# Kernel optimization log

Measured on AMD Instinct MI355X. Metric: run time of the kernel, lower is better.

Reference implementation:

```python
import jax, jax.numpy as jnp
import numpy as np

B, T, D_IN, H, LAT = 256, 512, 32, 128, 64


def lstm_scan(x, Wih, Whh, bih, bhh):
    """PyTorch-convention single-layer LSTM over x [B,T,D] -> hidden states [B,T,H].
    Gate order: i, f, g, o. Gates = x@Wih.T + bih + h@Whh.T + bhh."""
    Bm, _, _ = x.shape
    Hm = Whh.shape[1]
    # precompute input contributions for all timesteps: [B,T,4H]
    xg = jnp.einsum('btd,gd->btg', x, Wih) + bih + bhh

    def step(carry, g_t):
        h, c = carry
        gates = g_t + h @ Whh.T  # [B,4H]
        i, f, g, o = jnp.split(gates, 4, axis=-1)
        i = jax.nn.sigmoid(i)
        f = jax.nn.sigmoid(f)
        g = jnp.tanh(g)
        o = jax.nn.sigmoid(o)
        c = f * c + i * g
        h = o * jnp.tanh(c)
        return (h, c), h

    h0 = jnp.zeros((Bm, Hm), x.dtype)
    (_, _), hs = jax.lax.scan(step, (h0, h0), jnp.swapaxes(xg, 0, 1))
    return jnp.swapaxes(hs, 0, 1)  # [B,T,H]


def setup_inputs() -> dict:
    key = jax.random.key(0)
    ks = jax.random.split(key, 14)
    s = 1.0 / np.sqrt(H)

    def u(k, shape):
        return jax.random.uniform(k, shape, jnp.float32, -s, s)

    return {
        'x': jax.random.normal(ks[0], (B, T, D_IN), jnp.float32),
        # encoder LSTM (input_dim -> hidden)
        'enc_Wih': u(ks[1], (4 * H, D_IN)),
        'enc_Whh': u(ks[2], (4 * H, H)),
        'enc_bih': u(ks[3], (4 * H,)),
        'enc_bhh': u(ks[4], (4 * H,)),
        # encoder linear (hidden -> latent)
        'enc_Wl': u(ks[5], (LAT, H)),
        'enc_bl': u(ks[6], (LAT,)),
        # decoder LSTM (latent -> hidden)
        'dec_Wih': u(ks[7], (4 * H, LAT)),
        'dec_Whh': u(ks[8], (4 * H, H)),
        'dec_bih': u(ks[9], (4 * H,)),
        'dec_bhh': u(ks[10], (4 * H,)),
        # decoder linear (hidden -> input_dim)
        'dec_Wl': u(ks[11], (D_IN, H)),
        'dec_bl': u(ks[12], (D_IN,)),
    }


def reference(x, enc_Wih, enc_Whh, enc_bih, enc_bhh, enc_Wl, enc_bl,
              dec_Wih, dec_Whh, dec_bih, dec_bhh, dec_Wl, dec_bl):
    # Encoder: last hidden state -> linear -> latent
    hs = lstm_scan(x, enc_Wih, enc_Whh, enc_bih, enc_bhh)  # [B,T,H]
    h_last = hs[:, -1]                                     # == hidden.squeeze(0)
    encoded = h_last @ enc_Wl.T + enc_bl                   # [B,LAT]
    # Decoder: repeat latent over time, LSTM, linear
    z = jnp.broadcast_to(encoded[:, None, :], (encoded.shape[0], T, encoded.shape[1]))
    hs2 = lstm_scan(z, dec_Wih, dec_Whh, dec_bih, dec_bhh)  # [B,T,H]
    decoded = hs2 @ dec_Wl.T + dec_bl                       # [B,T,D_IN]
    return encoded, decoded
```

## Files before the change

### kernel.cpp

```cpp
#include <hip/hip_runtime.h>

#define NB   256
#define NT   512
#define NDIN 32
#define NH   128
#define NLAT 64
#define HSTR 136

typedef float    f32x4 __attribute__((ext_vector_type(4)));
typedef _Float16 h2    __attribute__((ext_vector_type(2)));
typedef _Float16 h4    __attribute__((ext_vector_type(4)));

__device__ __forceinline__ float dot2(h2 a, h2 b, float c) {
  return __builtin_amdgcn_fdot2(a, b, c, false);
}
__device__ __forceinline__ h2 bc2(float v) { return __builtin_bit_cast(h2, v); }
__device__ __forceinline__ h2 pk2(float a, float b) { return h2{(_Float16)a, (_Float16)b}; }

#define NLOG2E 1.44269504f
__device__ __forceinline__ float tanh_f(float x) {
  float s = __builtin_amdgcn_rcpf(1.f + __builtin_amdgcn_exp2f(x * (-2.f * NLOG2E)));
  return fmaf(2.f, s, -1.f);
}

template <int CTRL>
__device__ __forceinline__ float dpp_mov(float v) {
  int p = __builtin_amdgcn_update_dpp(0, __builtin_bit_cast(int, v),
                                      CTRL, 0xF, 0xF, true);
  return __builtin_bit_cast(float, p);
}
#define QXOR1 0xB1
#define QXOR2 0x4E
#define QP1   0x39
#define QP2   0x4E
#define QP3   0x93
template <int CTRL>
__device__ __forceinline__ float qadd(float v) { return v + dpp_mov<CTRL>(v); }

__global__ __launch_bounds__(512, 1) void lstm_ae_kernel(
    const float* __restrict__ x,
    const float* __restrict__ eWih,
    const float* __restrict__ eWhh,
    const float* __restrict__ eBih,
    const float* __restrict__ eBhh,
    const float* __restrict__ eWl,
    const float* __restrict__ eBl,
    const float* __restrict__ dWih,
    const float* __restrict__ dWhh,
    const float* __restrict__ dBih,
    const float* __restrict__ dBhh,
    const float* __restrict__ dWl,
    const float* __restrict__ dBl,
    float* __restrict__ outE,
    float* __restrict__ outD)
{
  extern __shared__ __align__(16) char smem[];
  float*    encs = (float*)smem;
  _Float16* hs   = (_Float16*)(encs + NLAT);
  _Float16* hist = hs + 2 * NH;
  _Float16* xs   = hist;
  float*    gtmp = (float*)(hist + NT * HSTR);

  const int tid = threadIdx.x;
  const int b   = blockIdx.x;
  const int u   = tid >> 2;
  const int kc  = tid & 3;
  const bool writer = (kc == 0);
  const bool k0 = (kc & 1) != 0;
  const bool k1 = (kc & 2) != 0;
  const bool gth = (kc == 2);
  const float km = gth ? (-2.f * NLOG2E) : -NLOG2E;
  const float pa = gth ? 2.f : 1.f;
  const float pb = gth ? -1.f : 0.f;

  {
    const float4* xg = (const float4*)(x + (size_t)b * (NT * NDIN));
    h4* xo = (h4*)xs;
#pragma unroll
    for (int i = 0; i < 8; ++i) {
      int idx = i * 512 + tid;
      float4 v = xg[idx];
      xo[idx] = h4{(_Float16)v.x, (_Float16)v.y, (_Float16)v.z, (_Float16)v.w};
    }
  }

  h2 ew[64], dw[64], ewih[16];
  float binit[4];
#pragma unroll
  for (int g = 0; g < 4; ++g) {
    const int r = g * NH + u;
    const float4* p = (const float4*)(eWhh + (size_t)r * NH + 32 * kc);
#pragma unroll
    for (int j = 0; j < 8; ++j) {
      float4 v = p[j];
      ew[g * 16 + 2 * j]     = pk2(v.x, v.y);
      ew[g * 16 + 2 * j + 1] = pk2(v.z, v.w);
    }
    const float4* q = (const float4*)(eWih + (size_t)r * NDIN + 8 * kc);
    float4 v0 = q[0], v1 = q[1];
    ewih[g * 4 + 0] = pk2(v0.x, v0.y);
    ewih[g * 4 + 1] = pk2(v0.z, v0.w);
    ewih[g * 4 + 2] = pk2(v1.x, v1.y);
    ewih[g * 4 + 3] = pk2(v1.z, v1.w);
    float bsum = eBih[r] + eBhh[r];
    binit[g] = writer ? bsum : 0.f;
  }
  if (tid < 2 * NH) hs[tid] = (_Float16)0.f;
  float c = 0.f;
  __syncthreads();

#pragma unroll 1
  for (int t = 0; t < NT; ++t) {
    const float4* hp = (const float4*)(hs + (t & 1) * NH + 32 * kc);
    float4 h0 = hp[0], h1 = hp[1], h2v = hp[2], h3 = hp[3];
    float4 xv = *(const float4*)(xs + t * NDIN + 8 * kc);
    float zz[4];
#pragma unroll
    for (int g = 0; g < 4; ++g) {
      float A = binit[g];
      A = dot2(ew[g * 16 +  0], bc2(h0.x), A);
      A = dot2(ew[g * 16 +  1], bc2(h0.y), A);
      A = dot2(ew[g * 16 +  2], bc2(h0.z), A);
      A = dot2(ew[g * 16 +  3], bc2(h0.w), A);
      A = dot2(ew[g * 16 +  4], bc2(h1.x), A);
      A = dot2(ew[g * 16 +  5], bc2(h1.y), A);
      A = dot2(ew[g * 16 +  6], bc2(h1.z), A);
      A = dot2(ew[g * 16 +  7], bc2(h1.w), A);
      A = dot2(ew[g * 16 +  8], bc2(h2v.x), A);
      A = dot2(ew[g * 16 +  9], bc2(h2v.y), A);
      A = dot2(ew[g * 16 + 10], bc2(h2v.z), A);
      A = dot2(ew[g * 16 + 11], bc2(h2v.w), A);
      A = dot2(ew[g * 16 + 12], bc2(h3.x), A);
      A = dot2(ew[g * 16 + 13], bc2(h3.y), A);
      A = dot2(ew[g * 16 + 14], bc2(h3.z), A);
      A = dot2(ew[g * 16 + 15], bc2(h3.w), A);
      A = dot2(ewih[g * 4 + 0], bc2(xv.x), A);
      A = dot2(ewih[g * 4 + 1], bc2(xv.y), A);
      A = dot2(ewih[g * 4 + 2], bc2(xv.z), A);
      A = dot2(ewih[g * 4 + 3], bc2(xv.w), A);
      A = qadd<QXOR1>(A);
      A = qadd<QXOR2>(A);
      zz[g] = A;
    }
    float zl = k0 ? zz[1] : zz[0];
    float zh = k0 ? zz[3] : zz[2];
    float z  = k1 ? zh : zl;
    float a  = fmaf(pa, __builtin_amdgcn_rcpf(1.f + __builtin_amdgcn_exp2f(z * km)), pb);
    float vf = dpp_mov<QP1>(a);
    float vg = dpp_mov<QP2>(a);
    float vo = dpp_mov<QP3>(a);
    c = fmaf(vf, c, a * vg);
    float h = vo * tanh_f(c);
    if (writer) hs[((t + 1) & 1) * NH + u] = (_Float16)h;
    __syncthreads();
  }

  if (tid < NLAT) {
    const float4* p  = (const float4*)(eWl + (size_t)tid * NH);
    const float2* hh = (const float2*)hs;
    float a = eBl[tid];
#pragma unroll
    for (int r = 0; r < 32; ++r) {
      float4 wv = p[r];
      float2 hp = hh[r];
      h2 lov = bc2(hp.x), hiv = bc2(hp.y);
      a = fmaf((float)lov.x, wv.x, a); a = fmaf((float)lov.y, wv.y, a);
      a = fmaf((float)hiv.x, wv.z, a); a = fmaf((float)hiv.y, wv.w, a);
    }
    encs[tid] = a;
    outE[b * NLAT + tid] = a;
  }
#pragma unroll
  for (int g = 0; g < 4; ++g) {
    const int r = g * NH + u;
    const float4* p = (const float4*)(dWhh + (size_t)r * NH + 32 * kc);
#pragma unroll
    for (int j = 0; j < 8; ++j) {
      float4 v = p[j];
      dw[g * 16 + 2 * j]     = pk2(v.x, v.y);
      dw[g * 16 + 2 * j + 1] = pk2(v.z, v.w);
    }
  }
  __syncthreads();

  if (tid < 2 * NH) hs[tid] = (_Float16)0.f;
  {
    const float4* p  = (const float4*)(dWih + (size_t)tid * NLAT);
    const float4* e4 = (const float4*)encs;
    float a = dBih[tid] + dBhh[tid];
#pragma unroll
    for (int r = 0; r < 16; ++r) {
      float4 wv = p[r]; float4 ev = e4[r];
      a = fmaf(ev.x, wv.x, a); a = fmaf(ev.y, wv.y, a);
      a = fmaf(ev.z, wv.z, a); a = fmaf(ev.w, wv.w, a);
    }
    gtmp[tid] = a;
  }
  __syncthreads();
  float dinit[4];
#pragma unroll
  for (int g = 0; g < 4; ++g)
    dinit[g] = writer ? gtmp[g * NH + u] : 0.f;
  c = 0.f;

#pragma unroll 1
  for (int t = 0; t < NT; ++t) {
    const float4* hp = (const float4*)(hs + (t & 1) * NH + 32 * kc);
    float4 h0 = hp[0], h1 = hp[1], h2v = hp[2], h3 = hp[3];
    float zz[4];
#pragma unroll
    for (int g = 0; g < 4; ++g) {
      float A = dinit[g];
      A = dot2(dw[g * 16 +  0], bc2(h0.x), A);
      A = dot2(dw[g * 16 +  1], bc2(h0.y), A);
      A = dot2(dw[g * 16 +  2], bc2(h0.z), A);
      A = dot2(dw[g * 16 +  3], bc2(h0.w), A);
      A = dot2(dw[g * 16 +  4], bc2(h1.x), A);
      A = dot2(dw[g * 16 +  5], bc2(h1.y), A);
      A = dot2(dw[g * 16 +  6], bc2(h1.z), A);
      A = dot2(dw[g * 16 +  7], bc2(h1.w), A);
      A = dot2(dw[g * 16 +  8], bc2(h2v.x), A);
      A = dot2(dw[g * 16 +  9], bc2(h2v.y), A);
      A = dot2(dw[g * 16 + 10], bc2(h2v.z), A);
      A = dot2(dw[g * 16 + 11], bc2(h2v.w), A);
      A = dot2(dw[g * 16 + 12], bc2(h3.x), A);
      A = dot2(dw[g * 16 + 13], bc2(h3.y), A);
      A = dot2(dw[g * 16 + 14], bc2(h3.z), A);
      A = dot2(dw[g * 16 + 15], bc2(h3.w), A);
      A = qadd<QXOR1>(A);
      A = qadd<QXOR2>(A);
      zz[g] = A;
    }
    float zl = k0 ? zz[1] : zz[0];
    float zh = k0 ? zz[3] : zz[2];
    float z  = k1 ? zh : zl;
    float a  = fmaf(pa, __builtin_amdgcn_rcpf(1.f + __builtin_amdgcn_exp2f(z * km)), pb);
    float vf = dpp_mov<QP1>(a);
    float vg = dpp_mov<QP2>(a);
    float vo = dpp_mov<QP3>(a);
    c = fmaf(vf, c, a * vg);
    float h = vo * tanh_f(c);
    if (writer) {
      _Float16 hh = (_Float16)h;
      hs[((t + 1) & 1) * NH + u] = hh;
      hist[t * HSTR + u] = hh;
    }
    __syncthreads();
  }

  {
    const int col = tid & 31, rg = tid >> 5;
    h2 wl[64];
    const float4* p0 = (const float4*)(dWl + (size_t)col * NH);
#pragma unroll
    for (int f = 0; f < 32; ++f) {
      float4 v = p0[f];
      wl[2 * f] = pk2(v.x, v.y); wl[2 * f + 1] = pk2(v.z, v.w);
    }
    const float bo = dBl[col];
    float* op = outD + (size_t)b * (NT * NDIN);
#pragma unroll 1
    for (int i = 0; i < 32; ++i) {
      int r = rg + 16 * i;
      const float4* hp = (const float4*)(hist + r * HSTR);
      float s = 0.f;
#pragma unroll
      for (int j = 0; j < 16; ++j) {
        float4 hvv = hp[j];
        s = dot2(wl[4 * j + 0], bc2(hvv.x), s);
        s = dot2(wl[4 * j + 1], bc2(hvv.y), s);
        s = dot2(wl[4 * j + 2], bc2(hvv.z), s);
        s = dot2(wl[4 * j + 3], bc2(hvv.w), s);
      }
      op[(size_t)r * NDIN + col] = s + bo;
    }
  }
}

#define SMEM_BYTES (NLAT * 4 + 2 * NH * 2 + NT * HSTR * 2 + 512 * 4)

extern "C" void kernel_launch(void* const* d_in, const int* in_sizes, int n_in,
                              void* d_out, int out_size, void* d_ws, size_t ws_size,
                              hipStream_t stream) {
  const float* x    = (const float*)d_in[0];
  const float* eWih = (const float*)d_in[1];
  const float* eWhh = (const float*)d_in[2];
  const float* eBih = (const float*)d_in[3];
  const float* eBhh = (const float*)d_in[4];
  const float* eWl  = (const float*)d_in[5];
  const float* eBl  = (const float*)d_in[6];
  const float* dWih = (const float*)d_in[7];
  const float* dWhh = (const float*)d_in[8];
  const float* dBih = (const float*)d_in[9];
  const float* dBhh = (const float*)d_in[10];
  const float* dWl  = (const float*)d_in[11];
  const float* dBl  = (const float*)d_in[12];

  float* outE = (float*)d_out;
  float* outD = outE + (size_t)NB * NLAT;

  (void)hipFuncSetAttribute((const void*)lstm_ae_kernel,
                            hipFuncAttributeMaxDynamicSharedMemorySize,
                            SMEM_BYTES);

  hipLaunchKernelGGL(lstm_ae_kernel, dim3(NB), dim3(512), SMEM_BYTES, stream,
                     x, eWih, eWhh, eBih, eBhh, eWl, eBl,
                     dWih, dWhh, dBih, dBhh, dWl, dBl, outE, outD);
}
```

Before: 625.1 us.

## Split each hidden unit's recurrent dot product across eight lanes with 1024 threads

Doubles the block to 1024 threads so each hidden unit's gate dot products are split over 8 lanes instead of 4. This halves the per-lane dot2 chain and register-held weights, with one extra DPP row-rotate step in the reduction. The encoder input projection for the next step is now computed after the hidden-state write, ahead of the barrier, taking it off the critical recurrent chain. The trade-off is a barrier across twice as many waves on every timestep and an extra cross-lane reduction stage.

```diff
diff --git a/kernel.cpp b/kernel.cpp
--- a/kernel.cpp
+++ b/kernel.cpp
@@ -31,13 +31,14 @@
 }
 #define QXOR1 0xB1
 #define QXOR2 0x4E
+#define ROR12 0x12C
 #define QP1   0x39
 #define QP2   0x4E
 #define QP3   0x93
 template <int CTRL>
 __device__ __forceinline__ float qadd(float v) { return v + dpp_mov<CTRL>(v); }
 
-__global__ __launch_bounds__(512, 1) void lstm_ae_kernel(
+__global__ __launch_bounds__(1024, 4) void lstm_ae_kernel(
     const float* __restrict__ x,
     const float* __restrict__ eWih,
     const float* __restrict__ eWhh,
@@ -63,12 +64,13 @@
 
   const int tid = threadIdx.x;
   const int b   = blockIdx.x;
-  const int u   = tid >> 2;
-  const int kc  = tid & 3;
+  const int u   = tid >> 3;
+  const int kc  = tid & 7;
+  const int kcq = kc & 3;
   const bool writer = (kc == 0);
-  const bool k0 = (kc & 1) != 0;
-  const bool k1 = (kc & 2) != 0;
-  const bool gth = (kc == 2);
+  const bool k0 = (kcq & 1) != 0;
+  const bool k1 = (kcq & 2) != 0;
+  const bool gth = (kcq == 2);
   const float km = gth ? (-2.f * NLOG2E) : -NLOG2E;
   const float pa = gth ? 2.f : 1.f;
   const float pb = gth ? -1.f : 0.f;
@@ -77,31 +79,29 @@
     const float4* xg = (const float4*)(x + (size_t)b * (NT * NDIN));
     h4* xo = (h4*)xs;
 #pragma unroll
-    for (int i = 0; i < 8; ++i) {
-      int idx = i * 512 + tid;
+    for (int i = 0; i < 4; ++i) {
+      int idx = i * 1024 + tid;
       float4 v = xg[idx];
       xo[idx] = h4{(_Float16)v.x, (_Float16)v.y, (_Float16)v.z, (_Float16)v.w};
     }
   }
 
-  h2 ew[64], dw[64], ewih[16];
+  h2 ew[32], dw[32], ewih[8];
   float binit[4];
 #pragma unroll
   for (int g = 0; g < 4; ++g) {
     const int r = g * NH + u;
-    const float4* p = (const float4*)(eWhh + (size_t)r * NH + 32 * kc);
-#pragma unroll
-    for (int j = 0; j < 8; ++j) {
+    const float4* p = (const float4*)(eWhh + (size_t)r * NH + 16 * kc);
+#pragma unroll
+    for (int j = 0; j < 4; ++j) {
       float4 v = p[j];
-      ew[g * 16 + 2 * j]     = pk2(v.x, v.y);
-      ew[g * 16 + 2 * j + 1] = pk2(v.z, v.w);
-    }
-    const float4* q = (const float4*)(eWih + (size_t)r * NDIN + 8 * kc);
-    float4 v0 = q[0], v1 = q[1];
-    ewih[g * 4 + 0] = pk2(v0.x, v0.y);
-    ewih[g * 4 + 1] = pk2(v0.z, v0.w);
-    ewih[g * 4 + 2] = pk2(v1.x, v1.y);
-    ewih[g * 4 + 3] = pk2(v1.z, v1.w);
+      ew[g * 8 + 2 * j]     = pk2(v.x, v.y);
+      ew[g * 8 + 2 * j + 1] = pk2(v.z, v.w);
+    }
+    const float4* q = (const float4*)(eWih + (size_t)r * NDIN + 4 * kc);
+    float4 v0 = q[0];
+    ewih[g * 2 + 0] = pk2(v0.x, v0.y);
+    ewih[g * 2 + 1] = pk2(v0.z, v0.w);
     float bsum = eBih[r] + eBhh[r];
     binit[g] = writer ? bsum : 0.f;
   }
@@ -109,37 +109,38 @@
   float c = 0.f;
   __syncthreads();
 
+  float xacc[4];
+  {
+    float2 xw = *(const float2*)(xs + 4 * kc);
+    h2 x0 = bc2(xw.x), x1 = bc2(xw.y);
+#pragma unroll
+    for (int g = 0; g < 4; ++g) {
+      float A = binit[g];
+      A = dot2(ewih[g * 2 + 0], x0, A);
+      A = dot2(ewih[g * 2 + 1], x1, A);
+      xacc[g] = A;
+    }
+  }
+
 #pragma unroll 1
   for (int t = 0; t < NT; ++t) {
-    const float4* hp = (const float4*)(hs + (t & 1) * NH + 32 * kc);
-    float4 h0 = hp[0], h1 = hp[1], h2v = hp[2], h3 = hp[3];
-    float4 xv = *(const float4*)(xs + t * NDIN + 8 * kc);
+    const float4* hp = (const float4*)(hs + (t & 1) * NH + 16 * kc);
+    float4 h0 = hp[0], h1 = hp[1];
     float zz[4];
 #pragma unroll
     for (int g = 0; g < 4; ++g) {
-      float A = binit[g];
-      A = dot2(ew[g * 16 +  0], bc2(h0.x), A);
-      A = dot2(ew[g * 16 +  1], bc2(h0.y), A);
-      A = dot2(ew[g * 16 +  2], bc2(h0.z), A);
-      A = dot2(ew[g * 16 +  3], bc2(h0.w), A);
-      A = dot2(ew[g * 16 +  4], bc2(h1.x), A);
-      A = dot2(ew[g * 16 +  5], bc2(h1.y), A);
-      A = dot2(ew[g * 16 +  6], bc2(h1.z), A);
-      A = dot2(ew[g * 16 +  7], bc2(h1.w), A);
-      A = dot2(ew[g * 16 +  8], bc2(h2v.x), A);
-      A = dot2(ew[g * 16 +  9], bc2(h2v.y), A);
-      A = dot2(ew[g * 16 + 10], bc2(h2v.z), A);
-      A = dot2(ew[g * 16 + 11], bc2(h2v.w), A);
-      A = dot2(ew[g * 16 + 12], bc2(h3.x), A);
-      A = dot2(ew[g * 16 + 13], bc2(h3.y), A);
-      A = dot2(ew[g * 16 + 14], bc2(h3.z), A);
-      A = dot2(ew[g * 16 + 15], bc2(h3.w), A);
-      A = dot2(ewih[g * 4 + 0], bc2(xv.x), A);
-      A = dot2(ewih[g * 4 + 1], bc2(xv.y), A);
-      A = dot2(ewih[g * 4 + 2], bc2(xv.z), A);
-      A = dot2(ewih[g * 4 + 3], bc2(xv.w), A);
+      float A = xacc[g];
+      A = dot2(ew[g * 8 + 0], bc2(h0.x), A);
+      A = dot2(ew[g * 8 + 1], bc2(h0.y), A);
+      A = dot2(ew[g * 8 + 2], bc2(h0.z), A);
+      A = dot2(ew[g * 8 + 3], bc2(h0.w), A);
+      A = dot2(ew[g * 8 + 4], bc2(h1.x), A);
+      A = dot2(ew[g * 8 + 5], bc2(h1.y), A);
+      A = dot2(ew[g * 8 + 6], bc2(h1.z), A);
+      A = dot2(ew[g * 8 + 7], bc2(h1.w), A);
       A = qadd<QXOR1>(A);
       A = qadd<QXOR2>(A);
+      A = qadd<ROR12>(A);
       zz[g] = A;
     }
     float zl = k0 ? zz[1] : zz[0];
@@ -152,6 +153,18 @@
     c = fmaf(vf, c, a * vg);
     float h = vo * tanh_f(c);
     if (writer) hs[((t + 1) & 1) * NH + u] = (_Float16)h;
+    {
+      int tn = (t + 1) & (NT - 1);
+      float2 xw = *(const float2*)(xs + tn * NDIN + 4 * kc);
+      h2 x0 = bc2(xw.x), x1 = bc2(xw.y);
+#pragma unroll
+      for (int g = 0; g < 4; ++g) {
+        float A = binit[g];
+        A = dot2(ewih[g * 2 + 0], x0, A);
+        A = dot2(ewih[g * 2 + 1], x1, A);
+        xacc[g] = A;
+      }
+    }
     __syncthreads();
   }
 
@@ -173,18 +186,18 @@
 #pragma unroll
   for (int g = 0; g < 4; ++g) {
     const int r = g * NH + u;
-    const float4* p = (const float4*)(dWhh + (size_t)r * NH + 32 * kc);
-#pragma unroll
-    for (int j = 0; j < 8; ++j) {
+    const float4* p = (const float4*)(dWhh + (size_t)r * NH + 16 * kc);
+#pragma unroll
+    for (int j = 0; j < 4; ++j) {
       float4 v = p[j];
-      dw[g * 16 + 2 * j]     = pk2(v.x, v.y);
-      dw[g * 16 + 2 * j + 1] = pk2(v.z, v.w);
+      dw[g * 8 + 2 * j]     = pk2(v.x, v.y);
+      dw[g * 8 + 2 * j + 1] = pk2(v.z, v.w);
     }
   }
   __syncthreads();
 
   if (tid < 2 * NH) hs[tid] = (_Float16)0.f;
-  {
+  if (tid < 512) {
     const float4* p  = (const float4*)(dWih + (size_t)tid * NLAT);
     const float4* e4 = (const float4*)encs;
     float a = dBih[tid] + dBhh[tid];
@@ -205,30 +218,23 @@
 
 #pragma unroll 1
   for (int t = 0; t < NT; ++t) {
-    const float4* hp = (const float4*)(hs + (t & 1) * NH + 32 * kc);
-    float4 h0 = hp[0], h1 = hp[1], h2v = hp[2], h3 = hp[3];
+    const float4* hp = (const float4*)(hs + (t & 1) * NH + 16 * kc);
+    float4 h0 = hp[0], h1 = hp[1];
     float zz[4];
 #pragma unroll
     for (int g = 0; g < 4; ++g) {
       float A = dinit[g];
-      A = dot2(dw[g * 16 +  0], bc2(h0.x), A);
-      A = dot2(dw[g * 16 +  1], bc2(h0.y), A);
-      A = dot2(dw[g * 16 +  2], bc2(h0.z), A);
-      A = dot2(dw[g * 16 +  3], bc2(h0.w), A);
-      A = dot2(dw[g * 16 +  4], bc2(h1.x), A);
-      A = dot2(dw[g * 16 +  5], bc2(h1.y), A);
-      A = dot2(dw[g * 16 +  6], bc2(h1.z), A);
-      A = dot2(dw[g * 16 +  7], bc2(h1.w), A);
-      A = dot2(dw[g * 16 +  8], bc2(h2v.x), A);
-      A = dot2(dw[g * 16 +  9], bc2(h2v.y), A);
-      A = dot2(dw[g * 16 + 10], bc2(h2v.z), A);
-      A = dot2(dw[g * 16 + 11], bc2(h2v.w), A);
-      A = dot2(dw[g * 16 + 12], bc2(h3.x), A);
-      A = dot2(dw[g * 16 + 13], bc2(h3.y), A);
-      A = dot2(dw[g * 16 + 14], bc2(h3.z), A);
-      A = dot2(dw[g * 16 + 15], bc2(h3.w), A);
+      A = dot2(dw[g * 8 + 0], bc2(h0.x), A);
+      A = dot2(dw[g * 8 + 1], bc2(h0.y), A);
+      A = dot2(dw[g * 8 + 2], bc2(h0.z), A);
+      A = dot2(dw[g * 8 + 3], bc2(h0.w), A);
+      A = dot2(dw[g * 8 + 4], bc2(h1.x), A);
+      A = dot2(dw[g * 8 + 5], bc2(h1.y), A);
+      A = dot2(dw[g * 8 + 6], bc2(h1.z), A);
+      A = dot2(dw[g * 8 + 7], bc2(h1.w), A);
       A = qadd<QXOR1>(A);
       A = qadd<QXOR2>(A);
+      A = qadd<ROR12>(A);
       zz[g] = A;
     }
     float zl = k0 ? zz[1] : zz[0];
@@ -260,8 +266,8 @@
     const float bo = dBl[col];
     float* op = outD + (size_t)b * (NT * NDIN);
 #pragma unroll 1
-    for (int i = 0; i < 32; ++i) {
-      int r = rg + 16 * i;
+    for (int i = 0; i < 16; ++i) {
+      int r = rg + 32 * i;
       const float4* hp = (const float4*)(hist + r * HSTR);
       float s = 0.f;
 #pragma unroll
@@ -303,7 +309,7 @@
                             hipFuncAttributeMaxDynamicSharedMemorySize,
                             SMEM_BYTES);
 
-  hipLaunchKernelGGL(lstm_ae_kernel, dim3(NB), dim3(512), SMEM_BYTES, stream,
+  hipLaunchKernelGGL(lstm_ae_kernel, dim3(NB), dim3(1024), SMEM_BYTES, stream,
                      x, eWih, eWhh, eBih, eBhh, eWl, eBl,
                      dWih, dWhh, dBih, dBhh, dWl, dBl, outE, outD);
 }
```

Measured after the change: 819.0 us. 31.0% more time.
